# Optimization experiments

Hardware: AMD Instinct MI355X
Metric: run time of the kernel (lower is better)

## Reference

```python
import jax, jax.numpy as jnp
import numpy as np
import math

# Module hyperparameters (match init_kwargs)
T_FRAMES = 12
LEN_Q = 8160          # sum_l H_l*W_l for levels (64,96),(32,48),(16,24),(8,12)
D_MODEL = 256
N_HEADS = 8
N_LEVELS = 4
T_WINDOW = 2
N_CURR = 4            # n_curr_points
N_TEMP = 2            # n_temporal_points
D_HEAD = D_MODEL // N_HEADS


def _offset_biases():
    """Replicates _reset_parameters() grid init for the offset biases."""
    thetas = np.arange(N_HEADS, dtype=np.float32) * (2.0 * math.pi / N_HEADS)
    grid = np.stack([np.cos(thetas), np.sin(thetas)], -1)            # (H, 2)
    grid = grid / np.abs(grid).max(-1, keepdims=True)
    curr = np.tile(grid.reshape(N_HEADS, 1, 1, 2), (1, N_LEVELS, N_CURR, 1))
    curr = curr * (np.arange(1, N_CURR + 1, dtype=np.float32).reshape(1, 1, N_CURR, 1))
    temp = np.tile(grid.reshape(N_HEADS, 1, 1, 1, 2), (1, N_LEVELS, T_WINDOW, N_TEMP, 1))
    temp = temp * (np.arange(1, N_TEMP + 1, dtype=np.float32).reshape(1, 1, 1, N_TEMP, 1))
    return jnp.asarray(curr.reshape(-1)), jnp.asarray(temp.reshape(-1))


def setup_inputs() -> dict:
    key = jax.random.key(0)
    ks = jax.random.split(key, 10)
    s = 0.02
    b_so, b_tso = _offset_biases()
    d_so = N_HEADS * N_LEVELS * N_CURR * 2          # 256
    d_aw = N_HEADS * N_LEVELS * N_CURR              # 128
    d_tso = N_HEADS * N_LEVELS * T_WINDOW * N_TEMP * 2  # 512
    d_taw = N_HEADS * N_LEVELS * T_WINDOW * N_TEMP      # 256
    return {
        "query": jax.random.normal(ks[0], (T_FRAMES, LEN_Q, D_MODEL), jnp.float32),
        "input_flatten": jax.random.normal(ks[1], (T_FRAMES, LEN_Q, D_MODEL), jnp.float32),
        "W_val": jax.random.normal(ks[2], (D_MODEL, D_MODEL), jnp.float32) * s,
        "b_val": jnp.zeros((D_MODEL,), jnp.float32),
        "W_so": jax.random.normal(ks[3], (D_MODEL, d_so), jnp.float32) * s,
        "b_so": b_so,
        "W_aw": jax.random.normal(ks[4], (D_MODEL, d_aw), jnp.float32) * s,
        "b_aw": jnp.zeros((d_aw,), jnp.float32),
        "W_tso": jax.random.normal(ks[5], (D_MODEL, d_tso), jnp.float32) * s,
        "b_tso": b_tso,
        "W_taw": jax.random.normal(ks[6], (D_MODEL, d_taw), jnp.float32) * s,
        "b_taw": jnp.zeros((d_taw,), jnp.float32),
    }


def reference(query, input_flatten, W_val, b_val, W_so, b_so, W_aw, b_aw,
              W_tso, b_tso, W_taw, b_taw):
    T, Lq, _ = query.shape
    # value projection -> (T, Len_in, H, D_head)
    value = (input_flatten @ W_val + b_val).reshape(T, -1, N_HEADS, D_HEAD)
    # current-frame sampling offsets -> (T, Lq, H, L, n_curr, 2)
    curr_off = (query @ W_so + b_so).reshape(T, Lq, N_HEADS, N_LEVELS, N_CURR, 2)
    # temporal sampling offsets -> (T, Lq, H, t_window*L, n_temp, 2) (flatten(3,4))
    temp_off = (query @ W_tso + b_tso).reshape(
        T, Lq, N_HEADS, T_WINDOW, N_LEVELS, N_TEMP, 2
    ).reshape(T, Lq, N_HEADS, T_WINDOW * N_LEVELS, N_TEMP, 2)
    # joint softmax over current + temporal attention logits
    caw = (query @ W_aw + b_aw).reshape(T, Lq, N_HEADS, N_LEVELS * N_CURR)
    taw = (query @ W_taw + b_taw).reshape(T, Lq, N_HEADS, T_WINDOW * N_LEVELS * N_TEMP)
    aw = jax.nn.softmax(jnp.concatenate([caw, taw], axis=-1), axis=-1)
    n_c = N_LEVELS * N_CURR
    aw_curr = aw[..., :n_c].reshape(T, Lq, N_HEADS, N_LEVELS, N_CURR)
    aw_temp = aw[..., n_c:].reshape(T, Lq, N_HEADS, T_WINDOW * N_LEVELS, N_TEMP)
    return (value, curr_off, temp_off, aw_curr, aw_temp)
```

## Files before the change

### kernel.cpp

```cpp
#include <hip/hip_runtime.h>
#include <stdint.h>

#define AS1 __attribute__((address_space(1)))
#define AS3 __attribute__((address_space(3)))

typedef __attribute__((ext_vector_type(8))) short short8;
typedef __attribute__((ext_vector_type(4))) float floatx4;

__device__ __forceinline__ unsigned short f2b_rne(float f) {
  union { float f; unsigned u; } c; c.f = f;
  unsigned u = c.u;
  unsigned r = u + 0x7fffu + ((u >> 16) & 1u);
  return (unsigned short)(r >> 16);
}

__global__ void prep_weights(const float* __restrict__ Wv,  const float* __restrict__ bv,
                             const float* __restrict__ Wso, const float* __restrict__ bso,
                             const float* __restrict__ Waw, const float* __restrict__ baw,
                             const float* __restrict__ Wtso,const float* __restrict__ btso,
                             const float* __restrict__ Wtaw,const float* __restrict__ btaw,
                             unsigned short* __restrict__ Wt, float* __restrict__ bcat) {
  int n = blockIdx.x;
  int k = threadIdx.x;
  const float* W; const float* b; int c, N;
  if (n < 256)      { W = Wv;   b = bv;   c = n;       N = 256; }
  else if (n < 512) { W = Wso;  b = bso;  c = n - 256; N = 256; }
  else if (n < 768) { W = Wtso; b = btso; c = n - 512; N = 256; }
  else if (n < 896) { W = Waw;  b = baw;  c = n - 768; N = 128; }
  else              { W = Wtaw; b = btaw; c = n - 896; N = 128; }
  Wt[n * 256 + k] = f2b_rne(W[(size_t)k * N + c]);
  if (k == 0) bcat[n] = b[c];
}

__global__ __launch_bounds__(256, 3)
void fused_all(const float* __restrict__ Q, const float* __restrict__ X,
               const unsigned short* __restrict__ Wt, const float* __restrict__ bcat,
               float* __restrict__ out, int M) {
  __shared__ __align__(16) char lds[49152];

  const int tid  = threadIdx.x;
  const int lane = tid & 63;
  const int wid  = tid >> 6;
  const int lrow = lane & 15;
  const int quad = lane >> 4;
  const int mw   = (wid >> 1) * 32;
  const int nw   = (wid & 1) * 64;
  const int mBase = blockIdx.x * 64;

#define STAGE_B(cur_, nt_, s_)                                                 \
  do {                                                                         \
    const unsigned short* Bb_ = Wt + (size_t)(nt_) * 128 * 256;                \
    _Pragma("unroll") for (int j = 0; j < 2; ++j) {                            \
      int ch = j * 256 + tid;                                                  \
      int r = ch >> 2, kc = ch & 3;                                            \
      int kcs = kc ^ ((r >> 1) & 3);            \
      const unsigned short* src = Bb_ + (size_t)r * 256 + (s_) * 32 + kcs * 8; \
      unsigned ldsoff = 32768u + (unsigned)(cur_) * 8192u +                    \
                        (unsigned)((j * 256 + (tid & ~63)) * 16);              \
      __builtin_amdgcn_global_load_lds((const AS1 void*)src,                   \
                                       (AS3 void*)(lds + ldsoff), 16, 0, 0);   \
    }                                                                          \
  } while (0)

  for (int phase = 0; phase < 2; ++phase) {
    const float* A = (phase == 0) ? X : Q;
    {
      floatx4 va[16];
#pragma unroll
      for (int i = 0; i < 16; ++i) {
        int id = i * 256 + tid;
        int r = id >> 6, c4 = id & 63;
        va[i] = *(const floatx4*)(A + (size_t)(mBase + r) * 256 + c4 * 4);
      }
#pragma unroll
      for (int i = 0; i < 16; ++i) {
        int id = i * 256 + tid;
        int r = id >> 6, c4 = id & 63;
        int c8 = c4 >> 1, hf = c4 & 1;
        int pos = (c8 & ~7) | ((c8 ^ r) & 7);
        uint2 pk;
        pk.x = ((unsigned)f2b_rne(va[i][1]) << 16) | f2b_rne(va[i][0]);
        pk.y = ((unsigned)f2b_rne(va[i][3]) << 16) | f2b_rne(va[i][2]);
        *(uint2*)(lds + r * 512 + pos * 16 + hf * 8) = pk;
      }
    }
    const int ntBase = phase ? 2 : 0;
    const int nT     = phase ? 4 : 2;
    const int T      = nT * 8;
    STAGE_B(0, ntBase, 0);
    __syncthreads();

    int cur = 0;
    for (int ntq = 0; ntq < nT; ++ntq) {
      const int nt = ntBase + ntq;
      floatx4 acc[2][4] = {};
      for (int s = 0; s < 8; ++s) {
        const int t = ntq * 8 + s;
        if (t + 1 < T) {
          const int nt2 = ntBase + ((t + 1) >> 3);
          const int s2  = (t + 1) & 7;
          STAGE_B(cur ^ 1, nt2, s2);
        }
        short8 af[2], bfr[4];
#pragma unroll
        for (int mi = 0; mi < 2; ++mi) {
          int row = mw + mi * 16 + lrow;
          int c8 = s * 4 + quad;
          int pos = (c8 & ~7) | ((c8 ^ row) & 7);
          af[mi] = *(const short8*)(lds + row * 512 + pos * 16);
        }
#pragma unroll
        for (int ni = 0; ni < 4; ++ni) {
          int r = nw + ni * 16 + lrow;
          bfr[ni] = *(const short8*)(lds + 32768 + cur * 8192 + r * 64 +
                                     ((quad ^ ((r >> 1) & 3)) * 16));
        }
#pragma unroll
        for (int mi = 0; mi < 2; ++mi)
#pragma unroll
          for (int ni = 0; ni < 4; ++ni)
            acc[mi][ni] = __builtin_amdgcn_mfma_f32_16x16x32_bf16(
                bfr[ni], af[mi], acc[mi][ni], 0, 0, 0);
        __builtin_amdgcn_sched_barrier(0);
        asm volatile("s_waitcnt vmcnt(0)" ::: "memory");
        __builtin_amdgcn_s_barrier();
        __builtin_amdgcn_sched_barrier(0);
        cur ^= 1;
      }
      const int seg = nt >> 1, halfn = nt & 1;
      float* O = out + (size_t)seg * ((size_t)M * 256) + halfn * 128;
#pragma unroll
      for (int ni = 0; ni < 4; ++ni) {
        floatx4 b4 = *(const floatx4*)(bcat + nt * 128 + nw + ni * 16 + quad * 4);
#pragma unroll
        for (int mi = 0; mi < 2; ++mi) {
          int row = mBase + mw + mi * 16 + lrow;
          *(floatx4*)(O + (size_t)row * 256 + nw + ni * 16 + quad * 4) =
              acc[mi][ni] + b4;
        }
      }
    }
  }
#undef STAGE_B

  const unsigned short* Wc  = Wt + (size_t)(768 + 32 * wid + lrow) * 256 + quad * 8;
  const unsigned short* Wtp = Wt + (size_t)(896 + 32 * wid + lrow) * 256 + quad * 8;
  floatx4 acc2[4][4] = {};
#pragma unroll
  for (int s = 0; s < 8; ++s) {
    short8 wa[4], qf[4];
    wa[0] = *(const short8*)(Wc + s * 32);
    wa[1] = *(const short8*)(Wc + 16 * 256 + s * 32);
    wa[2] = *(const short8*)(Wtp + s * 32);
    wa[3] = *(const short8*)(Wtp + 16 * 256 + s * 32);
#pragma unroll
    for (int qt = 0; qt < 4; ++qt) {
      int row = qt * 16 + lrow;
      int cg = s * 4 + quad;
      int pos = (cg & ~7) | ((cg ^ (row & 7)) & 7);
      qf[qt] = *(const short8*)(lds + row * 512 + pos * 16);
    }
#pragma unroll
    for (int qt = 0; qt < 4; ++qt)
#pragma unroll
      for (int t = 0; t < 4; ++t)
        acc2[qt][t] = __builtin_amdgcn_mfma_f32_16x16x32_bf16(
            wa[t], qf[qt], acc2[qt][t], 0, 0, 0);
  }

  float* awc = out + (size_t)3 * ((size_t)M * 256);
  float* awt = awc + (size_t)M * 128;
#pragma unroll
  for (int hp = 0; hp < 2; ++hp) {
    const int h = 2 * wid + hp;
    floatx4 bc = *(const floatx4*)(bcat + 768 + h * 16 + quad * 4);
    floatx4 bt = *(const floatx4*)(bcat + 896 + h * 16 + quad * 4);
#pragma unroll
    for (int qt = 0; qt < 4; ++qt) {
      float c0 = acc2[qt][hp][0] + bc[0];
      float c1 = acc2[qt][hp][1] + bc[1];
      float c2 = acc2[qt][hp][2] + bc[2];
      float c3 = acc2[qt][hp][3] + bc[3];
      float t0 = acc2[qt][2 + hp][0] + bt[0];
      float t1 = acc2[qt][2 + hp][1] + bt[1];
      float t2 = acc2[qt][2 + hp][2] + bt[2];
      float t3 = acc2[qt][2 + hp][3] + bt[3];
      float mx = fmaxf(fmaxf(fmaxf(c0, c1), fmaxf(c2, c3)),
                       fmaxf(fmaxf(t0, t1), fmaxf(t2, t3)));
      mx = fmaxf(mx, __shfl_xor(mx, 16));
      mx = fmaxf(mx, __shfl_xor(mx, 32));
      float e0 = __expf(c0 - mx), e1 = __expf(c1 - mx);
      float e2 = __expf(c2 - mx), e3 = __expf(c3 - mx);
      float f0 = __expf(t0 - mx), f1 = __expf(t1 - mx);
      float f2 = __expf(t2 - mx), f3 = __expf(t3 - mx);
      float sm = ((e0 + e1) + (e2 + e3)) + ((f0 + f1) + (f2 + f3));
      sm += __shfl_xor(sm, 16);
      sm += __shfl_xor(sm, 32);
      float inv = 1.0f / sm;
      int row = mBase + qt * 16 + lrow;
      floatx4 oc; oc[0] = e0 * inv; oc[1] = e1 * inv; oc[2] = e2 * inv; oc[3] = e3 * inv;
      floatx4 ot; ot[0] = f0 * inv; ot[1] = f1 * inv; ot[2] = f2 * inv; ot[3] = f3 * inv;
      *(floatx4*)(awc + (size_t)row * 128 + h * 16 + quad * 4) = oc;
      *(floatx4*)(awt + (size_t)row * 128 + h * 16 + quad * 4) = ot;
    }
  }
}

extern "C" void kernel_launch(void* const* d_in, const int* in_sizes, int n_in,
                              void* d_out, int out_size, void* d_ws, size_t ws_size,
                              hipStream_t stream) {
  const float* Q    = (const float*)d_in[0];
  const float* Xf   = (const float*)d_in[1];
  const float* Wv   = (const float*)d_in[2];
  const float* bv   = (const float*)d_in[3];
  const float* Wso  = (const float*)d_in[4];
  const float* bso  = (const float*)d_in[5];
  const float* Waw  = (const float*)d_in[6];
  const float* baw  = (const float*)d_in[7];
  const float* Wtso = (const float*)d_in[8];
  const float* btso = (const float*)d_in[9];
  const float* Wtaw = (const float*)d_in[10];
  const float* btaw = (const float*)d_in[11];
  float* out = (float*)d_out;

  unsigned short* Wt = (unsigned short*)d_ws;
  float* bcat = (float*)((char*)d_ws + 1024 * 256 * 2);

  int M = in_sizes[0] / 256;

  prep_weights<<<1024, 256, 0, stream>>>(Wv, bv, Wso, bso, Waw, baw,
                                         Wtso, btso, Wtaw, btaw, Wt, bcat);

  fused_all<<<M / 64, 256, 0, stream>>>(Q, Xf, Wt, bcat, out, M);
}
```

Baseline: 194.1 us.

## Give each wave private B staging to drop per-step block barriers

The warp tiling changes from a 2x2 (32 rows x 64 cols) split to each wave owning all 64 rows and a 32-column slice of the weight tile. Each wave now stages its own B slice into a private double-buffered LDS region with wave-local vmcnt waits, so the per-k-step __syncthreads-style barrier goes away. A barriers remain only around loading A. The cost is more A-fragment LDS reads per wave (4 instead of 2), and the prefetch restarts for each N-tile instead of running continuously.

```diff
diff --git a/kernel.cpp b/kernel.cpp
--- a/kernel.cpp
+++ b/kernel.cpp
@@ -43,27 +43,21 @@
   const int wid  = tid >> 6;
   const int lrow = lane & 15;
   const int quad = lane >> 4;
-  const int mw   = (wid >> 1) * 32;
-  const int nw   = (wid & 1) * 64;
+  const int nw32 = wid * 32;
   const int mBase = blockIdx.x * 64;
 
-#define STAGE_B(cur_, nt_, s_)                                                 \
-  do {                                                                         \
-    const unsigned short* Bb_ = Wt + (size_t)(nt_) * 128 * 256;                \
-    _Pragma("unroll") for (int j = 0; j < 2; ++j) {                            \
-      int ch = j * 256 + tid;                                                  \
-      int r = ch >> 2, kc = ch & 3;                                            \
-      int kcs = kc ^ ((r >> 1) & 3);            \
-      const unsigned short* src = Bb_ + (size_t)r * 256 + (s_) * 32 + kcs * 8; \
-      unsigned ldsoff = 32768u + (unsigned)(cur_) * 8192u +                    \
-                        (unsigned)((j * 256 + (tid & ~63)) * 16);              \
-      __builtin_amdgcn_global_load_lds((const AS1 void*)src,                   \
-                                       (AS3 void*)(lds + ldsoff), 16, 0, 0);   \
-    }                                                                          \
+  char* waveB = lds + 32768 + wid * 4096;
+  const int bchunk = (quad ^ ((lrow >> 2) & 3)) * 16;
+
+#define LDS_FENCE()                                        \
+  do {                                                     \
+    asm volatile("s_waitcnt lgkmcnt(0)" ::: "memory");     \
+    __builtin_amdgcn_sched_barrier(0);                     \
   } while (0)
 
   for (int phase = 0; phase < 2; ++phase) {
     const float* A = (phase == 0) ? X : Q;
+    if (phase == 1) __syncthreads();
     {
       floatx4 va[16];
 #pragma unroll
@@ -84,64 +78,84 @@
         *(uint2*)(lds + r * 512 + pos * 16 + hf * 8) = pk;
       }
     }
+    __syncthreads();
+
     const int ntBase = phase ? 2 : 0;
     const int nT     = phase ? 4 : 2;
-    const int T      = nT * 8;
-    STAGE_B(0, ntBase, 0);
-    __syncthreads();
-
-    int cur = 0;
     for (int ntq = 0; ntq < nT; ++ntq) {
       const int nt = ntBase + ntq;
-      floatx4 acc[2][4] = {};
+      const unsigned short* Bb = Wt + ((size_t)nt * 128 + nw32) * 256;
+      floatx4 acc[4][2] = {};
+
+#define STAGE_B(buf_, s_)                                                     \
+  do {                                                                        \
+    _Pragma("unroll") for (int j = 0; j < 2; ++j) {                           \
+      int ch = j * 64 + lane;                                                 \
+      int r_ = ch >> 2, kc = ch & 3;                                          \
+      int kcs = kc ^ ((r_ >> 2) & 3);                                         \
+      const unsigned short* src = Bb + (size_t)r_ * 256 + (s_) * 32 + kcs * 8;\
+      unsigned ldsoff = (unsigned)(32768 + wid * 4096 + (buf_) * 2048 +       \
+                                   j * 1024);                                 \
+      __builtin_amdgcn_global_load_lds((const AS1 void*)src,                  \
+                                       (AS3 void*)(lds + ldsoff), 16, 0, 0);  \
+    }                                                                         \
+  } while (0)
+
+      LDS_FENCE();
+      STAGE_B(0, 0);
+      __builtin_amdgcn_sched_barrier(0);
+      STAGE_B(1, 1);
+      __builtin_amdgcn_sched_barrier(0);
+#pragma unroll
       for (int s = 0; s < 8; ++s) {
-        const int t = ntq * 8 + s;
-        if (t + 1 < T) {
-          const int nt2 = ntBase + ((t + 1) >> 3);
-          const int s2  = (t + 1) & 7;
-          STAGE_B(cur ^ 1, nt2, s2);
-        }
-        short8 af[2], bfr[4];
-#pragma unroll
-        for (int mi = 0; mi < 2; ++mi) {
-          int row = mw + mi * 16 + lrow;
+        if (s < 7) {
+          asm volatile("s_waitcnt vmcnt(2)" ::: "memory");
+        } else {
+          asm volatile("s_waitcnt vmcnt(0)" ::: "memory");
+        }
+        __builtin_amdgcn_sched_barrier(0);
+        const int cur = s & 1;
+        short8 af[4], bfr[2];
+#pragma unroll
+        for (int mi = 0; mi < 4; ++mi) {
+          int row = mi * 16 + lrow;
           int c8 = s * 4 + quad;
           int pos = (c8 & ~7) | ((c8 ^ row) & 7);
           af[mi] = *(const short8*)(lds + row * 512 + pos * 16);
         }
 #pragma unroll
-        for (int ni = 0; ni < 4; ++ni) {
-          int r = nw + ni * 16 + lrow;
-          bfr[ni] = *(const short8*)(lds + 32768 + cur * 8192 + r * 64 +
-                                     ((quad ^ ((r >> 1) & 3)) * 16));
-        }
-#pragma unroll
-        for (int mi = 0; mi < 2; ++mi)
-#pragma unroll
-          for (int ni = 0; ni < 4; ++ni)
+        for (int ni = 0; ni < 2; ++ni)
+          bfr[ni] = *(const short8*)(waveB + cur * 2048 +
+                                     (ni * 16 + lrow) * 64 + bchunk);
+#pragma unroll
+        for (int mi = 0; mi < 4; ++mi)
+#pragma unroll
+          for (int ni = 0; ni < 2; ++ni)
             acc[mi][ni] = __builtin_amdgcn_mfma_f32_16x16x32_bf16(
                 bfr[ni], af[mi], acc[mi][ni], 0, 0, 0);
-        __builtin_amdgcn_sched_barrier(0);
-        asm volatile("s_waitcnt vmcnt(0)" ::: "memory");
-        __builtin_amdgcn_s_barrier();
-        __builtin_amdgcn_sched_barrier(0);
-        cur ^= 1;
-      }
+        if (s + 2 < 8) {
+          LDS_FENCE();
+          STAGE_B(cur, s + 2);
+          __builtin_amdgcn_sched_barrier(0);
+        }
+      }
+#undef STAGE_B
+
       const int seg = nt >> 1, halfn = nt & 1;
       float* O = out + (size_t)seg * ((size_t)M * 256) + halfn * 128;
 #pragma unroll
-      for (int ni = 0; ni < 4; ++ni) {
-        floatx4 b4 = *(const floatx4*)(bcat + nt * 128 + nw + ni * 16 + quad * 4);
-#pragma unroll
-        for (int mi = 0; mi < 2; ++mi) {
-          int row = mBase + mw + mi * 16 + lrow;
-          *(floatx4*)(O + (size_t)row * 256 + nw + ni * 16 + quad * 4) =
+      for (int ni = 0; ni < 2; ++ni) {
+        floatx4 b4 = *(const floatx4*)(bcat + nt * 128 + nw32 + ni * 16 + quad * 4);
+#pragma unroll
+        for (int mi = 0; mi < 4; ++mi) {
+          int row = mBase + mi * 16 + lrow;
+          *(floatx4*)(O + (size_t)row * 256 + nw32 + ni * 16 + quad * 4) =
               acc[mi][ni] + b4;
         }
       }
     }
   }
-#undef STAGE_B
+#undef LDS_FENCE
 
   const unsigned short* Wc  = Wt + (size_t)(768 + 32 * wid + lrow) * 256 + quad * 8;
   const unsigned short* Wtp = Wt + (size_t)(896 + 32 * wid + lrow) * 256 + quad * 8;
```

Result: faster. 187.3 us (-3.5%).
